# Optimization experiments

Hardware: AMD Instinct MI355X
Metric: run time of the kernel (lower is better)

Reference implementation:

```python
import jax, jax.numpy as jnp
import numpy as np
from math import sqrt

SIZE = 4096
NR_CORES = 2
RANK = 16
D = 64  # core_size: D**NR_CORES == SIZE


def setup_inputs() -> dict:
    key = jax.random.key(0)
    k_x, k_c0, k_c1, k_b = jax.random.split(key, 4)
    t = 1.0 / sqrt(SIZE)
    sigma = (t * sqrt(RANK) ** (1 - NR_CORES)) ** (1.0 / NR_CORES)
    x = jax.random.normal(k_x, (2, 4096, SIZE), dtype=jnp.float32)
    core0 = sigma * jax.random.normal(k_c0, (D, D, D, RANK, 1), dtype=jnp.float32)
    core1 = sigma * jax.random.normal(k_c1, (D, D, D, 1, RANK), dtype=jnp.float32)
    bias = sqrt(1.0 / SIZE) * jax.random.uniform(k_b, (SIZE,), minval=-1.0, maxval=1.0, dtype=jnp.float32)
    return {"x": x, "core0": core0, "core1": core1, "bias": bias}


def _btt_forward(x, cores, bias):
    d, c, size = D, NR_CORES, SIZE
    G = cores[0]  # (d,...,d, r, 1)
    for idx, core in enumerate(cores[1:]):
        j = d ** (idx + 1)
        i = d ** (c - idx - 1)
        core_r = core.reshape(j, d, i, core.shape[-2], core.shape[-1])
        G_r = G.reshape(j, d ** (idx + 1), i, G.shape[-2], G.shape[-1])
        # contract rank dim b: (j,x,i,cb) x (j,y,i,ba) -> (j,x,y,i,c,a)
        G = jnp.einsum('jxicb,jyiba->jxyica', core_r, G_r)
    G = G.reshape(size, size)
    out = x.reshape(-1, size) @ G + bias
    return out.reshape(x.shape)


def reference(x, core0, core1, bias):
    return _btt_forward(x, [core0, core1], bias)
```

## Files before the change

kernel.cpp:

```cpp
#include <hip/hip_runtime.h>
#include <hip/hip_bf16.h>
#include <stdint.h>
#include <stddef.h>

using bf16 = __hip_bfloat16;

typedef __attribute__((ext_vector_type(4))) float f32x4;
typedef __attribute__((ext_vector_type(16))) float f32x16;
typedef __attribute__((ext_vector_type(8))) short bf16x8;
typedef __attribute__((ext_vector_type(4))) unsigned short u16x4;

#define K_DIM 4096
#define M_ROWS 8192
#define BM 256
#define BN 256
#define BK 64
#define NT (K_DIM / BK)
#define MT2 (M_ROWS / BM)
#define NT2 (K_DIM / BN)

template<bool B> struct BC { static constexpr bool value = B; };

__global__ void conv_bf16(const float* __restrict__ in, bf16* __restrict__ outb, int n4) {
  int idx = blockIdx.x * blockDim.x + threadIdx.x;
  int stride = gridDim.x * blockDim.x;
  for (int k = idx; k < n4; k += stride) {
    f32x4 v = ((const f32x4*)in)[k];
    bf16 tmp[4];
    tmp[0] = __float2bfloat16(v.x);
    tmp[1] = __float2bfloat16(v.y);
    tmp[2] = __float2bfloat16(v.z);
    tmp[3] = __float2bfloat16(v.w);
    ((u16x4*)outb)[k] = *(const u16x4*)tmp;
  }
}

__global__ void build_gt(const float* __restrict__ core0, const float* __restrict__ core1,
                         bf16* __restrict__ GT) {
  int j = blockIdx.x >> 6;
  int i = blockIdx.x & 63;
  __shared__ float c0s[64][16];
  __shared__ float c1s[64][16];
  int t = threadIdx.x;
#pragma unroll
  for (int rep = 0; rep < 4; ++rep) {
    int idx = rep * 256 + t;
    int row = idx >> 4;
    int b = idx & 15;
    size_t base = ((size_t)(j * 64 + row) * 64 + i) * 16 + b;
    c1s[row][b] = core1[base];
    c0s[row][b] = core0[base];
  }
  __syncthreads();
  int x = t & 63;
  int ys = t >> 6;
  float r1[16];
#pragma unroll
  for (int b = 0; b < 16; ++b) r1[b] = c1s[x][b];
#pragma unroll
  for (int yy = 0; yy < 16; ++yy) {
    int y = ys * 16 + yy;
    float acc = 0.f;
#pragma unroll
    for (int b = 0; b < 16; ++b) acc += r1[b] * c0s[y][b];
    GT[((size_t)(y * 64 + i) << 12) + (size_t)(j * 64 + x)] = __float2bfloat16(acc);
  }
}

__device__ __forceinline__ void gload_lds16(const bf16* g, bf16* l) {
  __builtin_amdgcn_global_load_lds(
      (const __attribute__((address_space(1))) unsigned int*)(g),
      (__attribute__((address_space(3))) unsigned int*)(l),
      16, 0, 0);
}

#define BARRIER() __builtin_amdgcn_s_barrier()
#define SP1() __builtin_amdgcn_s_setprio(1)
#define SP0() __builtin_amdgcn_s_setprio(0)
#define VMCNT0() asm volatile("s_waitcnt vmcnt(0)" ::: "memory")

__global__ __launch_bounds__(512, 2)
void gemm_xg(const bf16* __restrict__ Xb, const bf16* __restrict__ GT,
             const float* __restrict__ bias, float* __restrict__ out) {
  __shared__ bf16 As[2][BM * BK];
  __shared__ bf16 Bs[2][BN * BK];

  int bid = blockIdx.x;
  int sb = (bid & 7) * (MT2 * NT2 / 8) + (bid >> 3);
  int bm = sb >> 4;
  int bn = sb & 15;

  int t = threadIdx.x;
  int lane = t & 63;
  int wid = t >> 6;

  int srow = t >> 3;
  int scol = t & 7;
  int sxor = scol ^ (srow & 7);
  const bf16* gA0 = Xb + ((size_t)(bm * BM + srow) * K_DIM) + sxor * 8;
  const bf16* gB0 = GT + ((size_t)(bn * BN + srow) * K_DIM) + sxor * 8;
  int lbase = srow * BK + scol * 8;

  auto sA = [&](int buf, int h, int kt) {
    const bf16* g = gA0 + (size_t)(h * 128) * K_DIM + (size_t)kt * BK;
    bf16* l = &As[buf][h * 128 * BK + lbase];
    gload_lds16(g, l);
    gload_lds16(g + (size_t)64 * K_DIM, l + 64 * BK);
  };
  auto sB = [&](int buf, int h, int kt) {
    const bf16* g = gB0 + (size_t)(h * 128) * K_DIM + (size_t)kt * BK;
    bf16* l = &Bs[buf][h * 128 * BK + lbase];
    gload_lds16(g, l);
    gload_lds16(g + (size_t)64 * K_DIM, l + 64 * BK);
  };

  int wm = wid >> 2;
  int wn = wid & 3;
  int l31 = lane & 31;
  int lh = lane >> 5;
  int x7 = l31 & 7;
  int abase = (wm * 128 + l31) * BK;
  int bbase = (wn * 64 + l31) * BK;
  int so[4];
#pragma unroll
  for (int s = 0; s < 4; ++s) so[s] = (((2 * s + lh) ^ x7) << 3);

  f32x16 acc[4][2] = {};
  bf16x8 a0[4], b0[2], a1[4], b1[2];

  auto readset = [&](bf16x8 (&af)[4], bf16x8 (&bv)[2],
                     const bf16* Ab, const bf16* Bb, int s) {
    int sofs = so[s];
#pragma unroll
    for (int mi = 0; mi < 4; ++mi)
      af[mi] = *(const bf16x8*)&Ab[abase + mi * 2048 + sofs];
#pragma unroll
    for (int ni = 0; ni < 2; ++ni)
      bv[ni] = *(const bf16x8*)&Bb[bbase + ni * 2048 + sofs];
  };
  auto mstep = [&](bf16x8 (&af)[4], bf16x8 (&bv)[2]) {
    SP1();
#pragma unroll
    for (int mi = 0; mi < 4; ++mi)
#pragma unroll
      for (int ni = 0; ni < 2; ++ni)
        acc[mi][ni] = __builtin_amdgcn_mfma_f32_32x32x16_bf16(
            af[mi], bv[ni], acc[mi][ni], 0, 0, 0);
    SP0();
  };

  const bf16* A0 = &As[0][0];
  const bf16* B0 = &Bs[0][0];
  const bf16* A1 = &As[1][0];
  const bf16* B1 = &Bs[1][0];

  auto tile = [&](int kt, const bf16* Ac, const bf16* Bc, int obuf, auto lastc) {
    constexpr bool LAST = decltype(lastc)::value;
    if (!LAST) { sA(obuf, 0, kt + 1); sA(obuf, 1, kt + 1); }
    readset(a1, b1, Ac, Bc, 1);
    mstep(a0, b0);
    if (!LAST) { sB(obuf, 0, kt + 1); sB(obuf, 1, kt + 1); }
    readset(a0, b0, Ac, Bc, 2);
    mstep(a1, b1);
    readset(a1, b1, Ac, Bc, 3);
    mstep(a0, b0);
    VMCNT0();
    mstep(a1, b1);
    BARRIER();
  };

  sA(0, 0, 0); sA(0, 1, 0);
  sB(0, 0, 0); sB(0, 1, 0);
  VMCNT0();
  BARRIER();
  readset(a0, b0, A0, B0, 0);

#pragma unroll 1
  for (int i = 0; i < NT / 2 - 1; ++i) {
    tile(2 * i, A0, B0, 1, BC<false>{});
    readset(a0, b0, A1, B1, 0);
    tile(2 * i + 1, A1, B1, 0, BC<false>{});
    readset(a0, b0, A0, B0, 0);
  }
  tile(NT - 2, A0, B0, 1, BC<false>{});
  readset(a0, b0, A1, B1, 0);
  tile(NT - 1, A1, B1, 0, BC<true>{});

  int colbase = bn * BN + wn * 64 + l31;
  int rowbase = bm * BM + wm * 128 + 4 * lh;
#pragma unroll
  for (int ni = 0; ni < 2; ++ni) {
    int col = colbase + ni * 32;
    float bv = bias[col];
#pragma unroll
    for (int mi = 0; mi < 4; ++mi) {
#pragma unroll
      for (int r = 0; r < 16; ++r) {
        int row = rowbase + mi * 32 + (r & 3) + 8 * (r >> 2);
        out[(size_t)row * K_DIM + col] = acc[mi][ni][r] + bv;
      }
    }
  }
}

extern "C" void kernel_launch(void* const* d_in, const int* in_sizes, int n_in,
                              void* d_out, int out_size, void* d_ws, size_t ws_size,
                              hipStream_t stream) {
  const float* x     = (const float*)d_in[0];
  const float* core0 = (const float*)d_in[1];
  const float* core1 = (const float*)d_in[2];
  const float* bias  = (const float*)d_in[3];
  float* out = (float*)d_out;

  bf16* Xb = (bf16*)d_ws;
  bf16* GT = (bf16*)((char*)d_ws + (size_t)M_ROWS * K_DIM * sizeof(bf16));

  conv_bf16<<<2048, 256, 0, stream>>>(x, Xb, (M_ROWS * K_DIM) / 4);
  build_gt<<<4096, 256, 0, stream>>>(core0, core1, GT);
  gemm_xg<<<MT2 * NT2, 512, 0, stream>>>(Xb, GT, bias, out);
}
```

Measured before the change: 310.5 us.

## Add ping-pong barriers with partial lgkmcnt waits and prefetch next tile's first fragments

Puts workgroup barriers around each MFMA cluster so that the two co-resident wave groups alternate between memory and compute phases. Explicit lgkmcnt(6) waits with sched_barrier let the MFMAs start while the newest LDS fragment reads are still outstanding. The first fragment read of the next k-tile moves inside the tile, before its last MFMA batch, to overlap it. The cost is many more s_barrier instructions per k-tile, which can stall waves if the phases do not line up.

Result: slower. 336.1 us (+8.3%).

```diff
diff --git a/kernel.cpp b/kernel.cpp
--- a/kernel.cpp
+++ b/kernel.cpp
@@ -74,7 +74,15 @@
       16, 0, 0);
 }
 
-#define BARRIER() __builtin_amdgcn_s_barrier()
+#define BARRIER() asm volatile("s_barrier" ::: "memory")
+#define LGKM6() do { \
+    asm volatile("s_waitcnt lgkmcnt(6)" ::: "memory"); \
+    __builtin_amdgcn_sched_barrier(0); \
+  } while (0)
+#define LGKM0() do { \
+    asm volatile("s_waitcnt lgkmcnt(0)" ::: "memory"); \
+    __builtin_amdgcn_sched_barrier(0); \
+  } while (0)
 #define SP1() __builtin_amdgcn_s_setprio(1)
 #define SP0() __builtin_amdgcn_s_setprio(0)
 #define VMCNT0() asm volatile("s_waitcnt vmcnt(0)" ::: "memory")
@@ -121,31 +129,28 @@
   int x7 = l31 & 7;
   int abase = (wm * 128 + l31) * BK;
   int bbase = (wn * 64 + l31) * BK;
-  int so[4];
-#pragma unroll
-  for (int s = 0; s < 4; ++s) so[s] = (((2 * s + lh) ^ x7) << 3);
 
   f32x16 acc[4][2] = {};
   bf16x8 a0[4], b0[2], a1[4], b1[2];
 
-  auto readset = [&](bf16x8 (&af)[4], bf16x8 (&bv)[2],
-                     const bf16* Ab, const bf16* Bb, int s) {
-    int sofs = so[s];
+  auto readset = [&](bf16x8 (&av)[4], bf16x8 (&bv)[2],
+                     const bf16* Ab, const bf16* Bb, int ks) {
+    int sofs = ((2 * ks + lh) ^ x7) << 3;
 #pragma unroll
     for (int mi = 0; mi < 4; ++mi)
-      af[mi] = *(const bf16x8*)&Ab[abase + mi * 2048 + sofs];
+      av[mi] = *(const bf16x8*)&Ab[abase + mi * 2048 + sofs];
 #pragma unroll
     for (int ni = 0; ni < 2; ++ni)
       bv[ni] = *(const bf16x8*)&Bb[bbase + ni * 2048 + sofs];
   };
-  auto mstep = [&](bf16x8 (&af)[4], bf16x8 (&bv)[2]) {
+  auto mfma8 = [&](bf16x8 (&av)[4], bf16x8 (&bv)[2]) {
     SP1();
 #pragma unroll
     for (int mi = 0; mi < 4; ++mi)
 #pragma unroll
       for (int ni = 0; ni < 2; ++ni)
         acc[mi][ni] = __builtin_amdgcn_mfma_f32_32x32x16_bf16(
-            af[mi], bv[ni], acc[mi][ni], 0, 0, 0);
+            av[mi], bv[ni], acc[mi][ni], 0, 0, 0);
     SP0();
   };
 
@@ -154,19 +159,38 @@
   const bf16* A1 = &As[1][0];
   const bf16* B1 = &Bs[1][0];
 
-  auto tile = [&](int kt, const bf16* Ac, const bf16* Bc, int obuf, auto lastc) {
+  auto tile = [&](int kt, const bf16* Ac, const bf16* Bc,
+                  const bf16* An, const bf16* Bn, int nb, auto lastc) {
     constexpr bool LAST = decltype(lastc)::value;
-    if (!LAST) { sA(obuf, 0, kt + 1); sA(obuf, 1, kt + 1); }
+
+    if (!LAST) { sA(nb, 0, kt + 1); sA(nb, 1, kt + 1); }
     readset(a1, b1, Ac, Bc, 1);
-    mstep(a0, b0);
-    if (!LAST) { sB(obuf, 0, kt + 1); sB(obuf, 1, kt + 1); }
+    BARRIER(); LGKM6();
+    mfma8(a0, b0);
+    BARRIER();
+
+    if (!LAST) { sB(nb, 0, kt + 1); sB(nb, 1, kt + 1); }
     readset(a0, b0, Ac, Bc, 2);
-    mstep(a1, b1);
+    BARRIER(); LGKM6();
+    mfma8(a1, b1);
+    BARRIER();
+
     readset(a1, b1, Ac, Bc, 3);
-    mstep(a0, b0);
-    VMCNT0();
-    mstep(a1, b1);
+    BARRIER(); LGKM6();
+    mfma8(a0, b0);
     BARRIER();
+
+    if (!LAST) {
+      VMCNT0();
+      BARRIER();
+      readset(a0, b0, An, Bn, 0);
+      LGKM6();
+      mfma8(a1, b1);
+      BARRIER();
+    } else {
+      BARRIER(); LGKM0();
+      mfma8(a1, b1);
+    }
   };
 
   sA(0, 0, 0); sA(0, 1, 0);
@@ -177,14 +201,11 @@
 
 #pragma unroll 1
   for (int i = 0; i < NT / 2 - 1; ++i) {
-    tile(2 * i, A0, B0, 1, BC<false>{});
-    readset(a0, b0, A1, B1, 0);
-    tile(2 * i + 1, A1, B1, 0, BC<false>{});
-    readset(a0, b0, A0, B0, 0);
-  }
-  tile(NT - 2, A0, B0, 1, BC<false>{});
-  readset(a0, b0, A1, B1, 0);
-  tile(NT - 1, A1, B1, 0, BC<true>{});
+    tile(2 * i,     A0, B0, A1, B1, 1, BC<false>{});
+    tile(2 * i + 1, A1, B1, A0, B0, 0, BC<false>{});
+  }
+  tile(NT - 2, A0, B0, A1, B1, 1, BC<false>{});
+  tile(NT - 1, A1, B1, A0, B0, 0, BC<true>{});
 
   int colbase = bn * BN + wn * 64 + l31;
   int rowbase = bm * BM + wm * 128 + 4 * lh;
```
